# Optimization experiments

Measured on AMD Instinct MI355X. Metric: run time of the kernel, lower is better.

Reference implementation:

```python
import jax, jax.numpy as jnp
import numpy as np

H = 1024          # hidden_size
NH = 16           # num_attention_heads
HD = H // NH      # head_dim = 64
FF = 4096         # intermediate_size
EPS = 1e-12       # layer_norm_eps
CLAMP = 1e9


def _layer_norm(x, gamma, beta):
    mu = jnp.mean(x, axis=-1, keepdims=True)
    var = jnp.mean(jnp.square(x - mu), axis=-1, keepdims=True)
    return (x - mu) * jax.lax.rsqrt(var + EPS) * gamma + beta


def setup_inputs() -> dict:
    key = jax.random.key(0)
    ks = jax.random.split(key, 12)
    B, S = 4, 2048
    s_h = 1.0 / np.sqrt(H)
    s_f = 1.0 / np.sqrt(FF)
    return {
        "hidden_states": jax.random.normal(ks[0], (B, S, H), jnp.float32),
        "Wq": jax.random.normal(ks[1], (H, H), jnp.float32) * s_h,
        "bq": jnp.zeros((H,), jnp.float32),
        "Wk": jax.random.normal(ks[2], (H, H), jnp.float32) * s_h,
        "bk": jnp.zeros((H,), jnp.float32),
        "Wv": jax.random.normal(ks[3], (H, H), jnp.float32) * s_h,
        "bv": jnp.zeros((H,), jnp.float32),
        "ln1_g": jnp.ones((H,), jnp.float32),
        "ln1_b": jnp.zeros((H,), jnp.float32),
        "W1": jax.random.normal(ks[4], (H, FF), jnp.float32) * s_h,
        "b1": jnp.zeros((FF,), jnp.float32),
        "W2": jax.random.normal(ks[5], (FF, H), jnp.float32) * s_f,
        "b2": jnp.zeros((H,), jnp.float32),
        "ln2_g": jnp.ones((H,), jnp.float32),
        "ln2_b": jnp.zeros((H,), jnp.float32),
    }


def reference(hidden_states, Wq, bq, Wk, bk, Wv, bv, ln1_g, ln1_b,
              W1, b1, W2, b2, ln2_g, ln2_b):
    B, S, _ = hidden_states.shape
    # QKV projections -> [B, NH, S, HD]
    def heads(x):
        return x.reshape(B, S, NH, HD).transpose(0, 2, 1, 3)
    q = heads(hidden_states @ Wq + bq)
    k = heads(hidden_states @ Wk + bk)
    v = heads(hidden_states @ Wv + bv)
    # manual attention: scale, clamp, softmax + 1e-9 epsilon
    scores = jnp.einsum('bhqd,bhkd->bhqk', q, k) / np.sqrt(HD)
    scores = jnp.clip(scores, -CLAMP, CLAMP)
    probs = jax.nn.softmax(scores, axis=-1) + 1e-9
    ctx = jnp.einsum('bhqk,bhkd->bhqd', probs, v)
    ctx = ctx.transpose(0, 2, 1, 3).reshape(B, S, NH * HD)
    # residual + LN (no output projection in this module)
    x = _layer_norm(hidden_states + ctx, ln1_g, ln1_b)
    # FFN with exact gelu + clamp
    inter = jax.nn.gelu(x @ W1 + b1, approximate=False)
    inter = jnp.clip(inter, -CLAMP, CLAMP)
    out = inter @ W2 + b2
    return _layer_norm(out + x, ln2_g, ln2_b)
```

## Files before the change

kernel.cpp:

```cpp
#include <hip/hip_runtime.h>
#include <math.h>


#define H_   1024
#define NH_  16
#define HD_  64
#define FF_  4096
#define S_   2048
#define B_   4
#define BS_  (B_ * S_)

#define EPI_NONE 0
#define EPI_GELU 1
#define EPI_QKV3 2

typedef unsigned short ushort_t;
typedef short v8s __attribute__((ext_vector_type(8)));
typedef float v4f __attribute__((ext_vector_type(4)));
typedef float v16f __attribute__((ext_vector_type(16)));

#define CQ_ 0.18033688011112042f

__device__ __forceinline__ unsigned short f2bf(float f) {
    union { float f; unsigned int u; } v; v.f = f;
    unsigned int u = v.u;
    return (unsigned short)((u + 0x7fffu + ((u >> 16) & 1u)) >> 16);
}
__device__ __forceinline__ float bf2f(unsigned short h) {
    union { unsigned int u; float f; } v; v.u = ((unsigned int)h) << 16;
    return v.f;
}

__device__ __forceinline__ unsigned cvt_pk_bf16(float lo, float hi) {
    unsigned r;
    asm("v_cvt_pk_bf16_f32 %0, %1, %2" : "=v"(r) : "v"(lo), "v"(hi));
    return r;
}
__device__ __forceinline__ void pl32_swap(unsigned &a, unsigned &b) {
    asm("v_permlane32_swap_b32 %0, %1" : "+v"(a), "+v"(b));
}

typedef __attribute__((address_space(1))) void gvoid;
typedef __attribute__((address_space(3))) void lvoid;
__device__ __forceinline__ void async16(const void* g, void* l) {
    __builtin_amdgcn_global_load_lds((gvoid*)g, (lvoid*)l, 16, 0, 0);
}

__device__ __forceinline__ float gelu_fast(float x) {
    const float x2 = x * x;
    const float w  = fmaf(x2, 0.044715f, 1.0f);
    const float e  = __builtin_exp2f(x * w * -2.3022083f);
    return x * __builtin_amdgcn_rcpf(1.0f + e);
}

__global__ __launch_bounds__(256)
void cast_bf16_kernel(const float* __restrict__ x, ushort_t* __restrict__ y)
{
    const size_t i = ((size_t)blockIdx.x * 256 + threadIdx.x) * 4;
    float4 v = *(const float4*)&x[i];
    ushort4 o;
    o.x = f2bf(v.x); o.y = f2bf(v.y); o.z = f2bf(v.z); o.w = f2bf(v.w);
    *(ushort4*)&y[i] = o;
}

__global__ __launch_bounds__(256)
void cast_transpose_kernel(const float* __restrict__ W, ushort_t* __restrict__ Wt,
                           int K, int N)
{
    __shared__ float tile[32][33];
    const int tid = threadIdx.x;
    const int n0 = blockIdx.x * 32, k0 = blockIdx.y * 32;
    const int r  = tid >> 3;
    const int c4 = (tid & 7) * 4;
    float4 v = *(const float4*)&W[(size_t)(k0 + r) * N + n0 + c4];
    tile[r][c4 + 0] = v.x; tile[r][c4 + 1] = v.y;
    tile[r][c4 + 2] = v.z; tile[r][c4 + 3] = v.w;
    __syncthreads();
    ushort4 o;
    o.x = f2bf(tile[c4 + 0][r]); o.y = f2bf(tile[c4 + 1][r]);
    o.z = f2bf(tile[c4 + 2][r]); o.w = f2bf(tile[c4 + 3][r]);
    *(ushort4*)&Wt[(size_t)(n0 + r) * K + k0 + c4] = o;
}

__global__ __launch_bounds__(256)
void concat3_kernel(const float* __restrict__ a, const float* __restrict__ b,
                    const float* __restrict__ c, float* __restrict__ o)
{
    const int i = blockIdx.x * 256 + threadIdx.x;
    o[i] = (i < 1024) ? a[i] : (i < 2048) ? b[i - 1024] : c[i - 2048];
}

template <int EPI>
__global__ __launch_bounds__(256)
void bgemm_kernel(const ushort_t* __restrict__ A, const ushort_t* __restrict__ Bt,
                  const float* __restrict__ bias, void* __restrict__ Cout,
                  int M, int N, int K)
{
    __shared__ ushort_t Atile[3 * 128 * 32];
    __shared__ ushort_t Btile[3 * 128 * 32];

    const int tid  = threadIdx.x;
    const int wave = tid >> 6;
    const int lane = tid & 63;
    const int m    = lane & 31;
    const int hi   = lane >> 5;
    const int wm   = wave >> 1, wn = wave & 1;
    const int blockM = blockIdx.y * 128;
    const int blockN = blockIdx.x * 128;

    v16f acc[2][2];
#pragma unroll
    for (int a = 0; a < 2; ++a)
#pragma unroll
        for (int b = 0; b < 2; ++b) acc[a][b] = (v16f)0.f;

    auto stage = [&](int buf, int ktile) {
        const int kt = ktile * 32;
#pragma unroll
        for (int i = 0; i < 2; ++i) {
            const int chunk = i * 256 + tid;
            const int row = chunk >> 2;
            const int g   = (chunk & 3) ^ (((row >> 1) ^ (row >> 3)) & 3);
            async16(A  + (size_t)(blockM + row) * K + kt + g * 8,
                    &Atile[buf * 4096 + chunk * 8]);
            async16(Bt + (size_t)(blockN + row) * K + kt + g * 8,
                    &Btile[buf * 4096 + chunk * 8]);
        }
    };

    const int sw = ((m >> 1) ^ (m >> 3)) & 3;
    auto compute = [&](int buf) {
        v8s af[2][2], bfr[2][2];
#pragma unroll
        for (int w = 0; w < 2; ++w) {
            const int slot = ((w * 2 + hi) ^ sw) * 8;
#pragma unroll
            for (int f = 0; f < 2; ++f) {
                af[w][f]  = *(const v8s*)&Atile[buf * 4096 + (wm * 64 + f * 32 + m) * 32 + slot];
                bfr[w][f] = *(const v8s*)&Btile[buf * 4096 + (wn * 64 + f * 32 + m) * 32 + slot];
            }
        }
        __builtin_amdgcn_s_setprio(1);
#pragma unroll
        for (int w = 0; w < 2; ++w)
#pragma unroll
            for (int a = 0; a < 2; ++a)
#pragma unroll
                for (int b = 0; b < 2; ++b)
                    acc[a][b] = __builtin_amdgcn_mfma_f32_32x32x16_bf16(
                        af[w][a], bfr[w][b], acc[a][b], 0, 0, 0);
        __builtin_amdgcn_s_setprio(0);
    };

    const int NT = K >> 5;

    stage(0, 0);
    stage(1, 1);
    asm volatile("s_waitcnt vmcnt(4)" ::: "memory");
    __builtin_amdgcn_s_barrier();
    __builtin_amdgcn_sched_barrier(0);

    int bc = 0, bs = 2;
    for (int t = 0; t < NT; ++t) {
        const bool more = (t + 2 < NT);
        if (more) {
            stage(bs, t + 2);
            bs = (bs == 2) ? 0 : bs + 1;
        }
        compute(bc);
        bc = (bc == 2) ? 0 : bc + 1;
        if (t < NT - 1) {
            asm volatile("s_waitcnt lgkmcnt(0)" ::: "memory");
            if (more) asm volatile("s_waitcnt vmcnt(4)" ::: "memory");
            else      asm volatile("s_waitcnt vmcnt(0)" ::: "memory");
            __builtin_amdgcn_s_barrier();
            __builtin_amdgcn_sched_barrier(0);
        }
    }

#pragma unroll
    for (int im = 0; im < 2; ++im) {
#pragma unroll
        for (int in = 0; in < 2; ++in) {
            const int n  = blockN + wn * 64 + in * 32 + m;
            const float bn = bias[n];
            if (EPI == EPI_QKV3) {
                const int nn = n & 1023;
                const int hh = nn >> 6, dd = nn & 63;
                ushort_t* base = (ushort_t*)Cout + (size_t)(n >> 10) * ((size_t)BS_ * H_);
                if (n < 2048) {
                    const float sc = (n < 1024) ? CQ_ : 1.f;
#pragma unroll
                    for (int g = 0; g < 4; ++g)
#pragma unroll
                        for (int rr = 0; rr < 4; ++rr) {
                            const int mr = blockM + wm * 64 + im * 32 + g * 8 + hi * 4 + rr;
                            base[(((size_t)((mr >> 11) * NH_ + hh)) * S_ + (mr & 2047)) * HD_ + dd]
                                = f2bf((acc[im][in][g * 4 + rr] + bn) * sc);
                        }
                } else {
#pragma unroll
                    for (int g = 0; g < 4; ++g) {
                        const int m0 = blockM + wm * 64 + im * 32 + g * 8 + hi * 4;
                        ushort4 pk;
                        pk.x = f2bf(acc[im][in][g * 4 + 0] + bn);
                        pk.y = f2bf(acc[im][in][g * 4 + 1] + bn);
                        pk.z = f2bf(acc[im][in][g * 4 + 2] + bn);
                        pk.w = f2bf(acc[im][in][g * 4 + 3] + bn);
                        *(ushort4*)&base[(((size_t)((m0 >> 11) * NH_ + hh)) * HD_ + dd) * S_
                                         + (m0 & 2047)] = pk;
                    }
                }
            } else {
#pragma unroll
                for (int g = 0; g < 4; ++g)
#pragma unroll
                    for (int rr = 0; rr < 4; ++rr) {
                        const int mr = blockM + wm * 64 + im * 32 + g * 8 + hi * 4 + rr;
                        float v = acc[im][in][g * 4 + rr] + bn;
                        if (EPI == EPI_GELU) {
                            ((ushort_t*)Cout)[(size_t)mr * N + n] = f2bf(gelu_fast(v));
                        } else {
                            ((float*)Cout)[(size_t)mr * N + n] = v;
                        }
                    }
            }
        }
    }
}

__global__ __launch_bounds__(256)
void vsum_kernel(const ushort_t* __restrict__ VT, float* __restrict__ vsum)
{
    const int bh   = blockIdx.x;
    const int tid  = threadIdx.x;
    const int d    = tid >> 2;
    const int part = tid & 3;
    const ushort_t* p = VT + (size_t)bh * HD_ * S_ + (size_t)d * S_ + part * 512;
    float acc = 0.f;
    for (int i = 0; i < 512; i += 4) {
        ushort4 u = *(const ushort4*)&p[i];
        acc += (bf2f(u.x) + bf2f(u.y)) + (bf2f(u.z) + bf2f(u.w));
    }
    acc += __shfl_xor(acc, 1);
    acc += __shfl_xor(acc, 2);
    if (part == 0) vsum[bh * HD_ + d] = acc;
}

__global__ __launch_bounds__(256)
void flash_kernel(const ushort_t* __restrict__ Q, const ushort_t* __restrict__ Kg,
                  const ushort_t* __restrict__ VT, const float* __restrict__ vsum,
                  float* __restrict__ ctx)
{
    __shared__ ushort_t Qs[128 * 64];
    __shared__ ushort_t Ks[2][64 * 64];
    __shared__ ushort_t Vs[2][64 * 64];

    int wg = blockIdx.x;
    wg = (wg & 7) * 128 + (wg >> 3);
    const int bh = wg >> 4;
    const int q0 = (wg & 15) * 128;

    const int tid  = threadIdx.x;
    const int wave = tid >> 6;
    const int lane = tid & 63;
    const int m    = lane & 31;
    const int hi   = lane >> 5;

    const ushort_t* Qp = Q  + (size_t)bh * S_ * HD_ + (size_t)q0 * HD_;
    const ushort_t* Kp = Kg + (size_t)bh * S_ * HD_;
    const ushort_t* Vp = VT + (size_t)bh * HD_ * S_;

    auto stageKV = [&](int buf, int t) {
        const int kv0 = t * 64;
#pragma unroll
        for (int i = 0; i < 2; ++i) {
            const int ch = i * 256 + tid;
            const int row = ch >> 3, c = ch & 7;
            async16(Kp + (size_t)(kv0 + row) * HD_ + ((c ^ (row & 7)) * 8),
                    &Ks[buf][ch * 8]);
            async16(Vp + (size_t)row * S_ + kv0 + ((c ^ (row & 7)) * 8),
                    &Vs[buf][ch * 8]);
        }
    };

#pragma unroll
    for (int i = 0; i < 4; ++i) {
        const int ch = i * 256 + tid;
        const int row = ch >> 3, c = ch & 7;
        async16(Qp + (size_t)row * HD_ + ((c ^ (row & 7)) * 8), &Qs[ch * 8]);
    }
    stageKV(0, 0);
    asm volatile("s_waitcnt vmcnt(0)" ::: "memory");
    __builtin_amdgcn_s_barrier();
    __builtin_amdgcn_sched_barrier(0);

    v8s qf[4];
    {
        const int qrow = wave * 32 + m;
#pragma unroll
        for (int c = 0; c < 4; ++c)
            qf[c] = *(const v8s*)&Qs[qrow * 64 + (((2 * c + hi) ^ (qrow & 7)) * 8)];
    }

    v16f o0 = (v16f)0.f, o1 = (v16f)0.f;
    float lp0 = 0.f, lp1 = 0.f, lp2 = 0.f, lp3 = 0.f;
    v8s pf[4];

    const int NT = S_ / 64;
    for (int t = 0; t < NT; ++t) {
        const int b = t & 1;
        if (t + 1 < NT) stageKV(b ^ 1, t + 1);

#pragma unroll
        for (int a = 0; a < 2; ++a) {
            v16f z = (v16f)0.f;
            const int krow = a * 32 + m;
#pragma unroll
            for (int c = 0; c < 4; ++c) {
                v8s kf = *(const v8s*)&Ks[b][krow * 64 + (((2 * c + hi) ^ (m & 7)) * 8)];
                z = __builtin_amdgcn_mfma_f32_32x32x16_bf16(kf, qf[c], z, 0, 0, 0);
            }
            unsigned u[8];
#pragma unroll
            for (int mm = 0; mm < 8; ++mm) {
                const float plo = __builtin_exp2f(z[2 * mm]);
                const float phi = __builtin_exp2f(z[2 * mm + 1]);
                if ((mm & 3) == 0)      lp0 += plo + phi;
                else if ((mm & 3) == 1) lp1 += plo + phi;
                else if ((mm & 3) == 2) lp2 += plo + phi;
                else                    lp3 += plo + phi;
                u[mm] = cvt_pk_bf16(plo, phi);
            }
            pl32_swap(u[0], u[2]); pl32_swap(u[1], u[3]);
            pl32_swap(u[4], u[6]); pl32_swap(u[5], u[7]);
            union { unsigned w[4]; v8s s; } c0, c1;
            c0.w[0] = u[0]; c0.w[1] = u[1]; c0.w[2] = u[2]; c0.w[3] = u[3];
            c1.w[0] = u[4]; c1.w[1] = u[5]; c1.w[2] = u[6]; c1.w[3] = u[7];
            pf[2 * a]     = c0.s;
            pf[2 * a + 1] = c1.s;
        }

#pragma unroll
        for (int c = 0; c < 4; ++c) {
            const int sw = ((2 * c + hi) ^ (m & 7)) * 8;
            v8s vf0 = *(const v8s*)&Vs[b][m * 64 + sw];
            v8s vf1 = *(const v8s*)&Vs[b][(32 + m) * 64 + sw];
            o0 = __builtin_amdgcn_mfma_f32_32x32x16_bf16(vf0, pf[c], o0, 0, 0, 0);
            o1 = __builtin_amdgcn_mfma_f32_32x32x16_bf16(vf1, pf[c], o1, 0, 0, 0);
        }

        asm volatile("s_waitcnt lgkmcnt(0)" ::: "memory");
        asm volatile("s_waitcnt vmcnt(0)" ::: "memory");
        __builtin_amdgcn_s_barrier();
        __builtin_amdgcn_sched_barrier(0);
    }

    float l_r = (lp0 + lp1) + (lp2 + lp3);
    l_r += __shfl_xor(l_r, 32);
    const float linv = 1.f / l_r;

    const int bb = bh >> 4, hh = bh & 15;
    const int srow = q0 + wave * 32 + m;
    float* cp = ctx + ((size_t)(bb * S_ + srow)) * H_ + hh * HD_;
#pragma unroll
    for (int g = 0; g < 2; ++g) {
        const v16f& o = g ? o1 : o0;
#pragma unroll
        for (int rq = 0; rq < 4; ++rq) {
            const int d0 = g * 32 + rq * 8 + hi * 4;
            float4 vs4 = *(const float4*)&vsum[bh * HD_ + d0];
            float4 ov;
            ov.x = o[rq * 4 + 0] * linv + 1e-9f * vs4.x;
            ov.y = o[rq * 4 + 1] * linv + 1e-9f * vs4.y;
            ov.z = o[rq * 4 + 2] * linv + 1e-9f * vs4.z;
            ov.w = o[rq * 4 + 3] * linv + 1e-9f * vs4.w;
            *(float4*)&cp[d0] = ov;
        }
    }
}

template <bool WB>
__global__ __launch_bounds__(256)
void add_ln_kernel(const float* __restrict__ A, const float* __restrict__ Bv,
                   const float* __restrict__ gamma, const float* __restrict__ beta,
                   float* __restrict__ out, ushort_t* __restrict__ outb)
{
    const int row = blockIdx.x;
    const int tid = threadIdx.x;
    const float* a = A  + (size_t)row * H_;
    const float* b = Bv + (size_t)row * H_;

    float4 av = *(const float4*)&a[tid * 4];
    float4 bv = *(const float4*)&b[tid * 4];
    float x[4] = { av.x + bv.x, av.y + bv.y, av.z + bv.z, av.w + bv.w };

    float s  = x[0] + x[1] + x[2] + x[3];
    float s2 = x[0]*x[0] + x[1]*x[1] + x[2]*x[2] + x[3]*x[3];
#pragma unroll
    for (int off = 1; off < 64; off <<= 1) {
        s  += __shfl_xor(s,  off);
        s2 += __shfl_xor(s2, off);
    }
    __shared__ float rs[8];
    const int wave = tid >> 6, lane = tid & 63;
    if (lane == 0) { rs[wave] = s; rs[4 + wave] = s2; }
    __syncthreads();
    const float sum  = rs[0] + rs[1] + rs[2] + rs[3];
    const float sum2 = rs[4] + rs[5] + rs[6] + rs[7];
    const float mu   = sum * (1.f / H_);
    const float var  = sum2 * (1.f / H_) - mu * mu;
    const float rstd = rsqrtf(var + 1e-12f);

    float4 gv = *(const float4*)&gamma[tid * 4];
    float4 be = *(const float4*)&beta[tid * 4];
    float4 ov;
    ov.x = (x[0] - mu) * rstd * gv.x + be.x;
    ov.y = (x[1] - mu) * rstd * gv.y + be.y;
    ov.z = (x[2] - mu) * rstd * gv.z + be.z;
    ov.w = (x[3] - mu) * rstd * gv.w + be.w;
    *(float4*)&out[(size_t)row * H_ + tid * 4] = ov;
    if (WB) {
        ushort4 ob;
        ob.x = f2bf(ov.x); ob.y = f2bf(ov.y); ob.z = f2bf(ov.z); ob.w = f2bf(ov.w);
        *(ushort4*)&outb[(size_t)row * H_ + tid * 4] = ob;
    }
}

extern "C" void kernel_launch(void* const* d_in, const int* in_sizes, int n_in,
                              void* d_out, int out_size, void* d_ws, size_t ws_size,
                              hipStream_t stream)
{
    const float* hidden = (const float*)d_in[0];
    const float* Wq     = (const float*)d_in[1];
    const float* bq     = (const float*)d_in[2];
    const float* Wk     = (const float*)d_in[3];
    const float* bk     = (const float*)d_in[4];
    const float* Wv     = (const float*)d_in[5];
    const float* bv     = (const float*)d_in[6];
    const float* ln1_g  = (const float*)d_in[7];
    const float* ln1_b  = (const float*)d_in[8];
    const float* W1     = (const float*)d_in[9];
    const float* b1     = (const float*)d_in[10];
    const float* W2     = (const float*)d_in[11];
    const float* b2     = (const float*)d_in[12];
    const float* ln2_g  = (const float*)d_in[13];
    const float* ln2_b  = (const float*)d_in[14];

    char* ws = (char*)d_ws;
    const size_t MB = 1024 * 1024;
    ushort_t* Xb    = (ushort_t*)(ws + 0);
    ushort_t* x1b   = (ushort_t*)(ws + 0);
    ushort_t* Wqt   = (ushort_t*)(ws + 16 * MB);
    ushort_t* Wkt   = (ushort_t*)(ws + 18 * MB);
    ushort_t* Wvt   = (ushort_t*)(ws + 20 * MB);
    ushort_t* W1t   = (ushort_t*)(ws + 16 * MB);
    ushort_t* W2t   = (ushort_t*)(ws + 24 * MB);
    ushort_t* q     = (ushort_t*)(ws + 32 * MB);
    ushort_t* k     = (ushort_t*)(ws + 48 * MB);
    ushort_t* vt    = (ushort_t*)(ws + 64 * MB);
    float*    ctx   = (float*)(ws + 80 * MB);
    ushort_t* inter = (ushort_t*)(ws + 32 * MB);
    float*    bcat  = (float*)(ws + 96 * MB);
    float*    vsum  = (float*)(ws + 96 * MB + 16384);
    float*    out2  = (float*)(ws + 96 * MB);
    float*    x1    = (float*)(ws + 128 * MB);
    float*    out   = (float*)d_out;

    const dim3 blk(256);

    cast_bf16_kernel<<<dim3(BS_ * H_ / 1024), blk, 0, stream>>>(hidden, Xb);
    cast_transpose_kernel<<<dim3(32, 32),  blk, 0, stream>>>(Wq, Wqt, H_, H_);
    cast_transpose_kernel<<<dim3(32, 32),  blk, 0, stream>>>(Wk, Wkt, H_, H_);
    cast_transpose_kernel<<<dim3(32, 32),  blk, 0, stream>>>(Wv, Wvt, H_, H_);
    cast_transpose_kernel<<<dim3(32, 128), blk, 0, stream>>>(W2, W2t, FF_, H_);
    concat3_kernel<<<dim3(12), blk, 0, stream>>>(bq, bk, bv, bcat);

    bgemm_kernel<EPI_QKV3><<<dim3(24, 64), blk, 0, stream>>>(
        Xb, Wqt, bcat, q, BS_, 3 * H_, H_);

    cast_transpose_kernel<<<dim3(128, 32), blk, 0, stream>>>(W1, W1t, H_, FF_);

    vsum_kernel<<<dim3(B_ * NH_), blk, 0, stream>>>(vt, vsum);

    flash_kernel<<<dim3((S_ / 128) * (B_ * NH_)), blk, 0, stream>>>(q, k, vt, vsum, ctx);

    add_ln_kernel<true><<<dim3(BS_), blk, 0, stream>>>(hidden, ctx, ln1_g, ln1_b, x1, x1b);

    bgemm_kernel<EPI_GELU><<<dim3(32, 64), blk, 0, stream>>>(x1b, W1t, b1, inter, BS_, FF_, H_);

    bgemm_kernel<EPI_NONE><<<dim3(8, 64), blk, 0, stream>>>(inter, W2t, b2, out2, BS_, H_, FF_);

    add_ln_kernel<false><<<dim3(BS_), blk, 0, stream>>>(out2, x1, ln2_g, ln2_b, out, nullptr);
}
```

Measured before the change: 596.8 us.

## Pair GEMM k-tiles per barrier with 4-buffer ring; alias flash Q into KV smem

The GEMM main loop now stages two k-tiles at a time into a four-slot LDS ring and computes two tiles per barrier, halving the number of barriers at the cost of more LDS (64KB per block) and waiting for all outstanding loads (vmcnt(0)) rather than keeping one tile in flight. The flash attention kernel merges Q, K and V shared buffers into a single 32KB array. Q sits in the region later reused for the second KV buffer, after a barrier once Q fragments are in registers. This reduces LDS footprint to allow more resident workgroups, while the GEMM change may lower occupancy.

```diff
diff --git a/kernel.cpp b/kernel.cpp
--- a/kernel.cpp
+++ b/kernel.cpp
@@ -96,8 +96,8 @@
                   const float* __restrict__ bias, void* __restrict__ Cout,
                   int M, int N, int K)
 {
-    __shared__ ushort_t Atile[3 * 128 * 32];
-    __shared__ ushort_t Btile[3 * 128 * 32];
+    __shared__ ushort_t Atile[4 * 128 * 32];
+    __shared__ ushort_t Btile[4 * 128 * 32];
 
     const int tid  = threadIdx.x;
     const int wave = tid >> 6;
@@ -156,23 +156,20 @@
 
     stage(0, 0);
     stage(1, 1);
-    asm volatile("s_waitcnt vmcnt(4)" ::: "memory");
+    asm volatile("s_waitcnt vmcnt(0)" ::: "memory");
     __builtin_amdgcn_s_barrier();
     __builtin_amdgcn_sched_barrier(0);
 
-    int bc = 0, bs = 2;
-    for (int t = 0; t < NT; ++t) {
-        const bool more = (t + 2 < NT);
-        if (more) {
-            stage(bs, t + 2);
-            bs = (bs == 2) ? 0 : bs + 1;
-        }
-        compute(bc);
-        bc = (bc == 2) ? 0 : bc + 1;
-        if (t < NT - 1) {
+    for (int t = 0; t < NT; t += 2) {
+        if (t + 2 < NT) {
+            stage((t + 2) & 3, t + 2);
+            stage((t + 3) & 3, t + 3);
+        }
+        compute(t & 3);
+        compute((t + 1) & 3);
+        if (t + 2 < NT) {
             asm volatile("s_waitcnt lgkmcnt(0)" ::: "memory");
-            if (more) asm volatile("s_waitcnt vmcnt(4)" ::: "memory");
-            else      asm volatile("s_waitcnt vmcnt(0)" ::: "memory");
+            asm volatile("s_waitcnt vmcnt(0)" ::: "memory");
             __builtin_amdgcn_s_barrier();
             __builtin_amdgcn_sched_barrier(0);
         }
@@ -252,9 +249,7 @@
                   const ushort_t* __restrict__ VT, const float* __restrict__ vsum,
                   float* __restrict__ ctx)
 {
-    __shared__ ushort_t Qs[128 * 64];
-    __shared__ ushort_t Ks[2][64 * 64];
-    __shared__ ushort_t Vs[2][64 * 64];
+    __shared__ ushort_t smem[16384];
 
     int wg = blockIdx.x;
     wg = (wg & 7) * 128 + (wg >> 3);
@@ -271,16 +266,20 @@
     const ushort_t* Kp = Kg + (size_t)bh * S_ * HD_;
     const ushort_t* Vp = VT + (size_t)bh * HD_ * S_;
 
+    ushort_t* Qs = &smem[8192];
+
     auto stageKV = [&](int buf, int t) {
         const int kv0 = t * 64;
+        ushort_t* Ksb = &smem[buf * 8192];
+        ushort_t* Vsb = &smem[buf * 8192 + 4096];
 #pragma unroll
         for (int i = 0; i < 2; ++i) {
             const int ch = i * 256 + tid;
             const int row = ch >> 3, c = ch & 7;
             async16(Kp + (size_t)(kv0 + row) * HD_ + ((c ^ (row & 7)) * 8),
-                    &Ks[buf][ch * 8]);
+                    &Ksb[ch * 8]);
             async16(Vp + (size_t)row * S_ + kv0 + ((c ^ (row & 7)) * 8),
-                    &Vs[buf][ch * 8]);
+                    &Vsb[ch * 8]);
         }
     };
 
@@ -302,6 +301,9 @@
         for (int c = 0; c < 4; ++c)
             qf[c] = *(const v8s*)&Qs[qrow * 64 + (((2 * c + hi) ^ (qrow & 7)) * 8)];
     }
+    asm volatile("s_waitcnt lgkmcnt(0)" ::: "memory");
+    __builtin_amdgcn_s_barrier();
+    __builtin_amdgcn_sched_barrier(0);
 
     v16f o0 = (v16f)0.f, o1 = (v16f)0.f;
     float lp0 = 0.f, lp1 = 0.f, lp2 = 0.f, lp3 = 0.f;
@@ -311,6 +313,8 @@
     for (int t = 0; t < NT; ++t) {
         const int b = t & 1;
         if (t + 1 < NT) stageKV(b ^ 1, t + 1);
+        const ushort_t* Ksb = &smem[b * 8192];
+        const ushort_t* Vsb = &smem[b * 8192 + 4096];
 
 #pragma unroll
         for (int a = 0; a < 2; ++a) {
@@ -318,7 +322,7 @@
             const int krow = a * 32 + m;
 #pragma unroll
             for (int c = 0; c < 4; ++c) {
-                v8s kf = *(const v8s*)&Ks[b][krow * 64 + (((2 * c + hi) ^ (m & 7)) * 8)];
+                v8s kf = *(const v8s*)&Ksb[krow * 64 + (((2 * c + hi) ^ (m & 7)) * 8)];
                 z = __builtin_amdgcn_mfma_f32_32x32x16_bf16(kf, qf[c], z, 0, 0, 0);
             }
             unsigned u[8];
@@ -344,8 +348,8 @@
 #pragma unroll
         for (int c = 0; c < 4; ++c) {
             const int sw = ((2 * c + hi) ^ (m & 7)) * 8;
-            v8s vf0 = *(const v8s*)&Vs[b][m * 64 + sw];
-            v8s vf1 = *(const v8s*)&Vs[b][(32 + m) * 64 + sw];
+            v8s vf0 = *(const v8s*)&Vsb[m * 64 + sw];
+            v8s vf1 = *(const v8s*)&Vsb[(32 + m) * 64 + sw];
             o0 = __builtin_amdgcn_mfma_f32_32x32x16_bf16(vf0, pf[c], o0, 0, 0, 0);
             o1 = __builtin_amdgcn_mfma_f32_32x32x16_bf16(vf1, pf[c], o1, 0, 0, 0);
         }
```

Result: slower. 615.3 us (+3.1%).

## Alias Q and KV buffers in LDS, unroll flash loop, compute row sums via MFMA

Applied to the files above, without the earlier changes.

The flash attention kernel now uses one 32KB shared buffer. The Q tile is aliased onto the second K/V buffer after Q is moved into registers, which cuts LDS use from 48KB and should allow more resident workgroups. The KV loop is unrolled by two with ping-pong buffers and incrementing global pointers. The softmax denominator now comes from an extra MFMA against a ones vector instead of per-element VALU adds, and the PV MFMA block runs at raised wave priority. This trades extra matrix-core work for fewer vector ops. The denominator now sums bf16-rounded probabilities, which changes rounding slightly.

```diff
diff --git a/kernel.cpp b/kernel.cpp
--- a/kernel.cpp
+++ b/kernel.cpp
@@ -252,9 +252,7 @@
                   const ushort_t* __restrict__ VT, const float* __restrict__ vsum,
                   float* __restrict__ ctx)
 {
-    __shared__ ushort_t Qs[128 * 64];
-    __shared__ ushort_t Ks[2][64 * 64];
-    __shared__ ushort_t Vs[2][64 * 64];
+    __shared__ ushort_t smem[16384];
 
     int wg = blockIdx.x;
     wg = (wg & 7) * 128 + (wg >> 3);
@@ -271,26 +269,30 @@
     const ushort_t* Kp = Kg + (size_t)bh * S_ * HD_;
     const ushort_t* Vp = VT + (size_t)bh * HD_ * S_;
 
-    auto stageKV = [&](int buf, int t) {
-        const int kv0 = t * 64;
-#pragma unroll
-        for (int i = 0; i < 2; ++i) {
-            const int ch = i * 256 + tid;
-            const int row = ch >> 3, c = ch & 7;
-            async16(Kp + (size_t)(kv0 + row) * HD_ + ((c ^ (row & 7)) * 8),
-                    &Ks[buf][ch * 8]);
-            async16(Vp + (size_t)row * S_ + kv0 + ((c ^ (row & 7)) * 8),
-                    &Vs[buf][ch * 8]);
-        }
+    const int r_  = tid >> 3, c_ = tid & 7;
+    const int gsw = (c_ ^ (r_ & 7)) * 8;
+    const ushort_t* kg0 = Kp + (size_t)r_ * HD_ + gsw;
+    const ushort_t* kg1 = Kp + (size_t)(32 + r_) * HD_ + gsw;
+    const ushort_t* vg0 = Vp + (size_t)r_ * S_ + gsw;
+    const ushort_t* vg1 = Vp + (size_t)(32 + r_) * S_ + gsw;
+    const int ldk0 = tid * 8, ldk1 = (256 + tid) * 8;
+
+    auto STAGE = [&](int bufe) {
+        async16(kg0, &smem[bufe + ldk0]);
+        async16(kg1, &smem[bufe + ldk1]);
+        async16(vg0, &smem[bufe + 4096 + ldk0]);
+        async16(vg1, &smem[bufe + 4096 + ldk1]);
+        kg0 += 64 * HD_; kg1 += 64 * HD_;
+        vg0 += 64;       vg1 += 64;
     };
 
 #pragma unroll
     for (int i = 0; i < 4; ++i) {
         const int ch = i * 256 + tid;
         const int row = ch >> 3, c = ch & 7;
-        async16(Qp + (size_t)row * HD_ + ((c ^ (row & 7)) * 8), &Qs[ch * 8]);
-    }
-    stageKV(0, 0);
+        async16(Qp + (size_t)row * HD_ + ((c ^ (row & 7)) * 8), &smem[8192 + ch * 8]);
+    }
+    STAGE(0);
     asm volatile("s_waitcnt vmcnt(0)" ::: "memory");
     __builtin_amdgcn_s_barrier();
     __builtin_amdgcn_sched_barrier(0);
@@ -300,38 +302,34 @@
         const int qrow = wave * 32 + m;
 #pragma unroll
         for (int c = 0; c < 4; ++c)
-            qf[c] = *(const v8s*)&Qs[qrow * 64 + (((2 * c + hi) ^ (qrow & 7)) * 8)];
-    }
-
-    v16f o0 = (v16f)0.f, o1 = (v16f)0.f;
-    float lp0 = 0.f, lp1 = 0.f, lp2 = 0.f, lp3 = 0.f;
+            qf[c] = *(const v8s*)&smem[8192 + qrow * 64 + (((2 * c + hi) ^ (qrow & 7)) * 8)];
+    }
+    asm volatile("s_waitcnt lgkmcnt(0)" ::: "memory");
+    __builtin_amdgcn_s_barrier();
+    __builtin_amdgcn_sched_barrier(0);
+
+    v8s onesf;
+#pragma unroll
+    for (int j = 0; j < 8; ++j) onesf[j] = (short)0x3F80;
+
+    v16f o0 = (v16f)0.f, o1 = (v16f)0.f, ol = (v16f)0.f;
     v8s pf[4];
 
-    const int NT = S_ / 64;
-    for (int t = 0; t < NT; ++t) {
-        const int b = t & 1;
-        if (t + 1 < NT) stageKV(b ^ 1, t + 1);
-
+    auto COMPUTE = [&](int bufe) {
 #pragma unroll
         for (int a = 0; a < 2; ++a) {
             v16f z = (v16f)0.f;
-            const int krow = a * 32 + m;
 #pragma unroll
             for (int c = 0; c < 4; ++c) {
-                v8s kf = *(const v8s*)&Ks[b][krow * 64 + (((2 * c + hi) ^ (m & 7)) * 8)];
+                v8s kf = *(const v8s*)&smem[bufe + (a * 32 + m) * 64
+                                            + (((2 * c + hi) ^ (m & 7)) * 8)];
                 z = __builtin_amdgcn_mfma_f32_32x32x16_bf16(kf, qf[c], z, 0, 0, 0);
             }
             unsigned u[8];
 #pragma unroll
-            for (int mm = 0; mm < 8; ++mm) {
-                const float plo = __builtin_exp2f(z[2 * mm]);
-                const float phi = __builtin_exp2f(z[2 * mm + 1]);
-                if ((mm & 3) == 0)      lp0 += plo + phi;
-                else if ((mm & 3) == 1) lp1 += plo + phi;
-                else if ((mm & 3) == 2) lp2 += plo + phi;
-                else                    lp3 += plo + phi;
-                u[mm] = cvt_pk_bf16(plo, phi);
-            }
+            for (int mm = 0; mm < 8; ++mm)
+                u[mm] = cvt_pk_bf16(__builtin_exp2f(z[2 * mm]),
+                                    __builtin_exp2f(z[2 * mm + 1]));
             pl32_swap(u[0], u[2]); pl32_swap(u[1], u[3]);
             pl32_swap(u[4], u[6]); pl32_swap(u[5], u[7]);
             union { unsigned w[4]; v8s s; } c0, c1;
@@ -340,25 +338,37 @@
             pf[2 * a]     = c0.s;
             pf[2 * a + 1] = c1.s;
         }
-
+        __builtin_amdgcn_s_setprio(1);
 #pragma unroll
         for (int c = 0; c < 4; ++c) {
-            const int sw = ((2 * c + hi) ^ (m & 7)) * 8;
-            v8s vf0 = *(const v8s*)&Vs[b][m * 64 + sw];
-            v8s vf1 = *(const v8s*)&Vs[b][(32 + m) * 64 + sw];
+            const int sl = ((2 * c + hi) ^ (m & 7)) * 8;
+            v8s vf0 = *(const v8s*)&smem[bufe + 4096 + m * 64 + sl];
+            v8s vf1 = *(const v8s*)&smem[bufe + 4096 + (32 + m) * 64 + sl];
             o0 = __builtin_amdgcn_mfma_f32_32x32x16_bf16(vf0, pf[c], o0, 0, 0, 0);
             o1 = __builtin_amdgcn_mfma_f32_32x32x16_bf16(vf1, pf[c], o1, 0, 0, 0);
-        }
-
+            ol = __builtin_amdgcn_mfma_f32_32x32x16_bf16(onesf, pf[c], ol, 0, 0, 0);
+        }
+        __builtin_amdgcn_s_setprio(0);
+    };
+
+    auto SYNC = [&]() {
         asm volatile("s_waitcnt lgkmcnt(0)" ::: "memory");
         asm volatile("s_waitcnt vmcnt(0)" ::: "memory");
         __builtin_amdgcn_s_barrier();
         __builtin_amdgcn_sched_barrier(0);
-    }
-
-    float l_r = (lp0 + lp1) + (lp2 + lp3);
-    l_r += __shfl_xor(l_r, 32);
-    const float linv = 1.f / l_r;
+    };
+
+    const int NT = S_ / 64;
+    for (int t = 0; t < NT; t += 2) {
+        STAGE(8192);
+        COMPUTE(0);
+        SYNC();
+        if (t + 2 < NT) STAGE(0);
+        COMPUTE(8192);
+        if (t + 2 < NT) SYNC();
+    }
+
+    const float linv = 1.f / ol[0];
 
     const int bb = bh >> 4, hh = bh & 15;
     const int srow = q0 + wave * 32 + m;
```

Result: faster. 581.6 us (-2.5%).
